# Kernel optimization log

Hardware: AMD Instinct MI355X
Metric: run time of the kernel (lower is better)

The kernel has to match this reference:

```python
import jax, jax.numpy as jnp
import numpy as np

DIM, H, D = 2048, 16, 128
D_C, D_CQ, D_ROPE = 512, 1536, 64
B, T = 2, 2048


def _rope(t, cos, sin):
    # t: [..., T, D_ROPE]; cos/sin: [T, D_ROPE//2] broadcast over leading dims
    h = D_ROPE // 2
    t1, t2 = t[..., :h], t[..., h:]
    return jnp.concatenate([t1 * cos - t2 * sin, t2 * cos + t1 * sin], axis=-1)


def setup_inputs() -> dict:
    key = jax.random.key(0)
    ks = jax.random.split(key, 10)
    init = lambda k, shp, fan: (jax.random.normal(k, shp, jnp.float32) / np.sqrt(fan).astype(np.float32))
    x = jax.random.normal(ks[0], (B, T, DIM), jnp.float32)
    # RoPE tables for d_rope//2 = 32 rotary channels
    inv_freq = 1.0 / (10000.0 ** (np.arange(0, D_ROPE // 2, dtype=np.float32) / (D_ROPE // 2)))
    ang = np.arange(T, dtype=np.float32)[:, None] * inv_freq[None, :]
    cos = jnp.asarray(np.cos(ang), jnp.float32)
    sin = jnp.asarray(np.sin(ang), jnp.float32)
    return {
        "x": x,
        "cos": cos,
        "sin": sin,
        "w_kv": init(ks[1], (DIM, D_C), DIM),          # kv_compress
        "w_kdec": init(ks[2], (D_C, H * D), D_C),       # k_decompress
        "w_vdec": init(ks[3], (D_C, H * D), D_C),       # v_decompress
        "w_qc": init(ks[4], (DIM, D_CQ), DIM),          # q_compress
        "w_qdec": init(ks[5], (D_CQ, H * D), D_CQ),     # q_decompress
        "w_krope": init(ks[6], (DIM, D_ROPE), DIM),     # k_rope_proj
        "w_qrope": init(ks[7], (DIM, D_ROPE), DIM),     # q_rope_proj
        "w_o": init(ks[8], (H * D, DIM), H * D),        # wo
    }


def reference(x, cos, sin, w_kv, w_kdec, w_vdec, w_qc, w_qdec, w_krope, w_qrope, w_o):
    Bx, Tx, _ = x.shape
    # latent compress -> decompress
    c_kv = x @ w_kv                                       # [B,T,d_c]
    k = (c_kv @ w_kdec).reshape(Bx, Tx, H, D).transpose(0, 2, 1, 3)  # [B,H,T,D]
    v = (c_kv @ w_vdec).reshape(Bx, Tx, H, D).transpose(0, 2, 1, 3)
    c_q = x @ w_qc
    q = (c_q @ w_qdec).reshape(Bx, Tx, H, D).transpose(0, 2, 1, 3)
    # RoPE branch: head-shared projections, rotated then broadcast across heads
    k_rope = _rope(x @ w_krope, cos, sin)                 # [B,T,d_rope]
    q_rope = _rope(x @ w_qrope, cos, sin)
    rope_dim = min(D_ROPE, D)
    qr = jnp.broadcast_to(q_rope[:, None, :, :rope_dim], (Bx, H, Tx, rope_dim))
    kr = jnp.broadcast_to(k_rope[:, None, :, :rope_dim], (Bx, H, Tx, rope_dim))
    q = jnp.concatenate([q[..., :-rope_dim], qr], axis=-1)
    k = jnp.concatenate([k[..., :-rope_dim], kr], axis=-1)
    # causal SDPA, scale = 1/sqrt(head_dim)
    scores = jnp.einsum("bhtd,bhsd->bhts", q, k) / np.float32(np.sqrt(D))
    causal = jnp.tril(jnp.ones((Tx, Tx), dtype=bool))
    scores = jnp.where(causal, scores, jnp.float32(-1e30))
    attn = jax.nn.softmax(scores, axis=-1)
    out = jnp.einsum("bhts,bhsd->bhtd", attn, v)
    out = out.transpose(0, 2, 1, 3).reshape(Bx, Tx, H * D)
    return out @ w_o
```

## Files before the change

kernel.cpp:

```cpp
#include <hip/hip_runtime.h>
#include <stdint.h>
#include <math.h>

#define B_    2
#define T_    2048
#define DIM_  2048
#define H_    16
#define DC_   512
#define DCQ_  1536
#define NROWS (B_*T_)

typedef unsigned short u16;
typedef __attribute__((ext_vector_type(8))) __bf16 bf16x8;
typedef __attribute__((ext_vector_type(4))) float  f32x4;
typedef __attribute__((ext_vector_type(8))) unsigned short u16x8;
typedef __attribute__((ext_vector_type(4))) float  f4v;

__device__ __forceinline__ u16 f2bf(float f){
  unsigned u = __float_as_uint(f);
  u += 0x7FFFu + ((u >> 16) & 1u);
  return (u16)(u >> 16);
}
__device__ __forceinline__ float bf2f(u16 h){ return __uint_as_float(((unsigned)h) << 16); }

__device__ __forceinline__ unsigned cvt_pk_bf16(float lo, float hi){
  unsigned r;
  asm("v_cvt_pk_bf16_f32 %0, %1, %2" : "=v"(r) : "v"(lo), "v"(hi));
  return r;
}

__device__ __forceinline__ void gld_lds16(const void* g, void* l){
  auto gp = reinterpret_cast<__attribute__((address_space(1))) unsigned int*>(
      reinterpret_cast<uintptr_t>(g));
  auto lp = reinterpret_cast<__attribute__((address_space(3))) unsigned int*>(
      reinterpret_cast<uintptr_t>(l));
  __builtin_amdgcn_global_load_lds(gp, lp, 16, 0, 0);
}

__device__ __forceinline__ f32x4 mfma16(bf16x8 a, bf16x8 b, f32x4 c){
  return __builtin_amdgcn_mfma_f32_16x16x32_bf16(a, b, c, 0, 0, 0);
}

__device__ __forceinline__ void vmwait0(){ asm volatile("s_waitcnt vmcnt(0)" ::: "memory"); }
__device__ __forceinline__ void vmwait8(){ asm volatile("s_waitcnt vmcnt(8)" ::: "memory"); }
__device__ __forceinline__ void barr(){ asm volatile("s_barrier" ::: "memory"); }


struct TDesc { const void* src; u16* dst; int srcStride, dstStride, cblk, nbx, blk0; };
struct TPack { TDesc d[8]; };
#define CONVBLK 8192

__global__ void k_prep(const void* __restrict__ xsrc, u16* __restrict__ x_bf,
                       TPack p, const u16* __restrict__ cosr){
  __shared__ u16 tile[64][72];
  const int bid = blockIdx.x;
  const int tid = threadIdx.x;
  const int f = (cosr[0] == (u16)0x3F80u);
  if (bid < CONVBLK){
    if (f) return;
    int id = bid * 256 + tid;
    f4v v = reinterpret_cast<const f4v*>(xsrc)[id];
    unsigned lo = (unsigned)f2bf(v.x) | ((unsigned)f2bf(v.y) << 16);
    unsigned hi = (unsigned)f2bf(v.z) | ((unsigned)f2bf(v.w) << 16);
    reinterpret_cast<uint2*>(x_bf)[id] = make_uint2(lo, hi);
    return;
  }
  const int tb = bid - CONVBLK;
  int i = 0;
  #pragma unroll
  for (int k = 1; k < 8; ++k) if (tb >= p.d[k].blk0) i = k;
  const void* src = p.d[i].src;
  u16* dst = p.d[i].dst;
  const int srcStride = p.d[i].srcStride, dstStride = p.d[i].dstStride;
  const int rel = tb - p.d[i].blk0;
  const int bx = rel % p.d[i].nbx, by = rel / p.d[i].nbx;
  const int r0 = by << 6, c0 = bx * p.d[i].cblk;
  #pragma unroll
  for (int it = 0; it < 2; ++it){
    int task = (it << 8) + tid;
    int r = task >> 3, c8 = (task & 7) << 3;
    if (f){
      const u16* pp = (const u16*)src + (size_t)(r0 + r) * srcStride + c0 + c8;
      u16x8 v = *reinterpret_cast<const u16x8*>(pp);
      #pragma unroll
      for (int j = 0; j < 8; ++j) tile[r][c8 + j] = v[j];
    } else {
      const float* pp = (const float*)src + (size_t)(r0 + r) * srcStride + c0 + c8;
      f4v a = reinterpret_cast<const f4v*>(pp)[0];
      f4v b = reinterpret_cast<const f4v*>(pp)[1];
      tile[r][c8+0]=f2bf(a.x); tile[r][c8+1]=f2bf(a.y); tile[r][c8+2]=f2bf(a.z); tile[r][c8+3]=f2bf(a.w);
      tile[r][c8+4]=f2bf(b.x); tile[r][c8+5]=f2bf(b.y); tile[r][c8+6]=f2bf(b.z); tile[r][c8+7]=f2bf(b.w);
    }
  }
  __syncthreads();
  #pragma unroll
  for (int it = 0; it < 2; ++it){
    int task = (it << 8) + tid;
    int rr = task >> 3, cc8 = (task & 7) << 3;
    u16x8 v;
    #pragma unroll
    for (int j = 0; j < 8; ++j) v[j] = tile[cc8 + j][rr];
    *reinterpret_cast<u16x8*>(dst + (size_t)((bx << 6) + rr) * dstStride + r0 + cc8) = v;
  }
}

__global__ __launch_bounds__(256, 2) void k_gemm(
    const u16* __restrict__ A0, int lda0, const u16* __restrict__ Bt0, int K0,
    u16* __restrict__ C0, int ldc0, float os0,
    const u16* __restrict__ A1, int lda1, const u16* __restrict__ Bt1, int K1,
    u16* __restrict__ C1, int ldc1, float os1,
    int ysplit, int swz, void* outp, const u16* __restrict__ cosr,
    const u16* __restrict__ alt0, const u16* __restrict__ alt1,
    u16* __restrict__ vt0, u16* __restrict__ vt1,
    const u16* __restrict__ ropeXc, const void* __restrict__ rcosp,
    const void* __restrict__ rsinp, u16* __restrict__ ropeK,
    u16* __restrict__ ropeQ, int* __restrict__ rticket, int ngemm){
  __shared__ alignas(16) u16 lds[32768];
  const int tid = threadIdx.x;
  const int flat = blockIdx.y * gridDim.x + blockIdx.x;

  if (ropeXc && flat >= ngemm){
    const int rb = flat - ngemm;
    if (rb == 0 && tid < 128) rticket[tid] = 0;
    const int f2 = (((const u16*)rcosp)[0] == (u16)0x3F80u);
    int id = rb * 256 + tid;
    int row = id >> 7, c = id & 127;
    int t = row & (T_ - 1);
    int d = c & 63, i = d & 31;
    float cs, sn;
    if (f2){ cs = bf2f(((const u16*)rcosp)[t * 32 + i]); sn = bf2f(((const u16*)rsinp)[t * 32 + i]); }
    else   { cs = ((const float*)rcosp)[t * 32 + i];     sn = ((const float*)rsinp)[t * 32 + i]; }
    int base = c & 64;
    float t1 = bf2f(ropeXc[(size_t)row * 2304 + 2048 + base + i]);
    float t2 = bf2f(ropeXc[(size_t)row * 2304 + 2048 + base + 32 + i]);
    float v = (d < 32) ? (t1 * cs - t2 * sn) : (t2 * cs + t1 * sn);
    if (c >= 64) v *= 0.12753139626374414f;
    ((c < 64) ? ropeK : ropeQ)[(size_t)row * 64 + d] = f2bf(v);
    return;
  }

  const int wid = tid >> 6, lane = tid & 63;
  const int wr = wid >> 1, wc = wid & 1;
  const int l16 = lane & 15, g = lane >> 4;
  int lin = flat;
  if (swz){
    const int q8 = (gridDim.x * gridDim.y) >> 3;
    lin = (lin & 7) * q8 + (lin >> 3);
  }
  const int m0 = (lin & 31) << 7;
  int nt = lin >> 5;
  const u16 *A, *Bt, *alt; u16 *C, *vtp; int lda, K, ldc; float oscale;
  if (nt < ysplit){ A = A0; lda = lda0; Bt = Bt0; K = K0; C = C0; ldc = ldc0; oscale = os0; alt = alt0; vtp = vt0; }
  else { nt -= ysplit; A = A1; lda = lda1; Bt = Bt1; K = K1; C = C1; ldc = ldc1; oscale = os1; alt = alt1; vtp = vt1; }
  const int f = cosr ? (cosr[0] == (u16)0x3F80u) : 1;
  if (alt && f) A = alt;
  const int n0 = nt << 7;
  const size_t Kz = (size_t)K;
  const int nkt = K >> 6;

  auto STAGE = [&](int kt, int bufn){
    const int kb = kt << 6;
    #pragma unroll
    for (int q = 0; q < 8; ++q){
      const int ht = q >> 2;
      const int cq = ((q & 3) << 8) + tid;
      const int Lb = cq << 4;
      const int row = Lb >> 7;
      const int colb = (Lb & 127) ^ ((row & 7) << 4);
      const u16* src = ht ? (Bt + (size_t)(n0 + row) * Kz + kb + (colb >> 1))
                          : (A  + (size_t)(m0 + row) * lda + kb + (colb >> 1));
      gld_lds16(src, &lds[bufn * 16384 + ht * 8192 + (cq << 3)]);
    }
  };

  f32x4 acc[4][4] = {};

  STAGE(0, 0);
  int buf = 0;

  for (int kt = 0; kt < nkt; ++kt){
    if (kt + 1 < nkt){ STAGE(kt + 1, buf ^ 1); vmwait8(); }
    else vmwait0();
    barr();
    bf16x8 af[2][4], bfr[2][4];
    #pragma unroll
    for (int ks = 0; ks < 2; ++ks){
      #pragma unroll
      for (int mi = 0; mi < 4; ++mi){
        int row = (wr << 6) + (mi << 4) + l16;
        int cb = ((ks << 6) + (g << 4)) ^ ((row & 7) << 4);
        af[ks][mi] = *reinterpret_cast<const bf16x8*>(&lds[buf * 16384 + (((row << 7) + cb) >> 1)]);
      }
      #pragma unroll
      for (int ni = 0; ni < 4; ++ni){
        int row = (wc << 6) + (ni << 4) + l16;
        int cb = ((ks << 6) + (g << 4)) ^ ((row & 7) << 4);
        bfr[ks][ni] = *reinterpret_cast<const bf16x8*>(&lds[buf * 16384 + 8192 + (((row << 7) + cb) >> 1)]);
      }
    }
    __builtin_amdgcn_s_setprio(1);
    #pragma unroll
    for (int ks = 0; ks < 2; ++ks)
      #pragma unroll
      for (int mi = 0; mi < 4; ++mi)
        #pragma unroll
        for (int ni = 0; ni < 4; ++ni)
          acc[mi][ni] = mfma16(af[ks][mi], bfr[ks][ni], acc[mi][ni]);
    __builtin_amdgcn_s_setprio(0);
    barr();
    buf ^= 1;
  }

  const int r4 = g << 2;
  #pragma unroll
  for (int mi = 0; mi < 4; ++mi){
    int row = m0 + (wr << 6) + (mi << 4) + r4;
    #pragma unroll
    for (int ni = 0; ni < 4; ++ni){
      int col = n0 + (wc << 6) + (ni << 4) + l16;
      if (vtp && col >= 1024){
        int hd = col - 1024;
        u16* dst = vtp + (((size_t)(((row >> 11) << 4) + (hd >> 7)) << 7) + (hd & 127)) * (size_t)T_ + (row & (T_ - 1));
        union { u16 u[4]; uint2 v; } pk;
        #pragma unroll
        for (int j = 0; j < 4; ++j) pk.u[j] = f2bf(acc[mi][ni][j] * oscale);
        *reinterpret_cast<uint2*>(dst) = pk.v;
        continue;
      }
      #pragma unroll
      for (int j = 0; j < 4; ++j){
        float v = acc[mi][ni][j] * oscale;
        if (outp){
          if (f) ((u16*)outp)[(size_t)(row + j) * ldc + col] = f2bf(v);
          else   ((float*)outp)[(size_t)(row + j) * ldc + col] = v;
        } else {
          C[(size_t)(row + j) * ldc + col] = f2bf(v);
        }
      }
    }
  }
}

__global__ __launch_bounds__(512, 2) void k_attn(const u16* __restrict__ qP,
                                                 const u16* __restrict__ kvP,
                                                 const u16* __restrict__ vT,
                                                 const u16* __restrict__ krope,
                                                 const u16* __restrict__ qrope,
                                                 u16* __restrict__ aout,
                                                 int* __restrict__ ticket){
  __shared__ alignas(16) u16 smem[32768];
  const int tid = threadIdx.x, wid = tid >> 6, lane = tid & 63;
  const int l16 = lane & 15, g = lane >> 4;
  const int lk = g << 3, r4 = g << 2;
  const int sw8 = (l16 & 7) << 3;
  const int xcd = blockIdx.x & 7;

  while (true){
    if (tid == 0) *(int*)&smem[0] = atomicAdd(&ticket[xcd << 4], 1);
    __syncthreads();
    const int it = *(const int*)&smem[0];
    __syncthreads();
    if (it >= 64) break;
    const int qt = 15 - (it >> 2);
    const int bh = (xcd << 2) + (it & 3), b = bh >> 4, h = bh & 15;
    const int q0 = qt << 7;
    const size_t bT = (size_t)b * T_;
    const u16* kvPb = kvP + bT * 1024 + (h << 6);
    const u16* krb  = krope + bT * 64;
    const u16* vTb  = vT + (size_t)bh * 128 * T_;
    const int qlo = q0 + (wid << 4);
    const int qhi = qlo + 15;
    const int nkv = (qt << 1) + 2;

    auto STAGE = [&](int buf, int k0){
      const int base = buf << 14;
      #pragma unroll
      for (int r = 0; r < 4; ++r){
        int c = (r << 9) + tid;
        const u16* src;
        if (r < 2){
          int row = c >> 4, cc = c & 15;
          int ccx = (cc & 8) | ((cc & 7) ^ (row & 7));
          int col0 = ccx << 3;
          src = (col0 < 64) ? (kvPb + (size_t)(k0 + row) * 1024 + col0)
                            : (krb  + (size_t)(k0 + row) * 64 + (col0 - 64));
        } else {
          int cv = c - 1024;
          int row = cv >> 3, cc = cv & 7;
          int ccx = cc ^ (row & 7);
          src = vTb + (size_t)row * T_ + k0 + (ccx << 3);
        }
        gld_lds16(src, &smem[base + (c << 3)]);
      }
    };

    bf16x8 qf[4];
    {
      size_t grow = bT + qlo + l16;
      #pragma unroll
      for (int ks = 0; ks < 4; ++ks){
        int d = (ks << 5) + lk;
        const u16* src = (ks < 2) ? (qP + grow * 1024 + (h << 6) + d)
                                  : (qrope + grow * 64 + (d - 64));
        qf[ks] = *reinterpret_cast<const bf16x8*>(src);
      }
    }
    f32x4 o[8] = {};
    float m = -3e38f, l = 0.f;

    STAGE(0, 0);
    __syncthreads();
    int cur = 0;

    for (int kv = 0; kv < nkv; ++kv){
      const int k0 = kv << 6;
      if (kv + 1 < nkv) STAGE(cur ^ 1, (kv + 1) << 6);
      if (k0 <= qhi){
        const int kb = cur << 14;
        f32x4 s[4] = {};
        __builtin_amdgcn_s_setprio(1);
        #pragma unroll
        for (int ks = 0; ks < 4; ++ks){
          int colsw = ((ks << 5) + lk) ^ sw8;
          #pragma unroll
          for (int n = 0; n < 4; ++n){
            bf16x8 kf = *reinterpret_cast<const bf16x8*>(&smem[kb + ((n << 4) + l16) * 128 + colsw]);
            s[n] = mfma16(kf, qf[ks], s[n]);
          }
        }
        __builtin_amdgcn_s_setprio(0);
        if (k0 + 63 > qlo){
          const int tq = qlo + l16;
          #pragma unroll
          for (int n = 0; n < 4; ++n)
            #pragma unroll
            for (int j = 0; j < 4; ++j)
              s[n][j] = (k0 + (n << 4) + r4 + j <= tq) ? s[n][j] : -3e38f;
        }
        float mx;
        {
          float a0 = fmaxf(fmaxf(s[0][0], s[0][1]), fmaxf(s[0][2], s[0][3]));
          float a1 = fmaxf(fmaxf(s[1][0], s[1][1]), fmaxf(s[1][2], s[1][3]));
          float a2 = fmaxf(fmaxf(s[2][0], s[2][1]), fmaxf(s[2][2], s[2][3]));
          float a3 = fmaxf(fmaxf(s[3][0], s[3][1]), fmaxf(s[3][2], s[3][3]));
          mx = fmaxf(fmaxf(a0, a1), fmaxf(a2, a3));
          mx = fmaxf(mx, __shfl_xor(mx, 16));
          mx = fmaxf(mx, __shfl_xor(mx, 32));
        }
        if (__ballot(mx > m + 8.f)){
          float mnew = fmaxf(m, mx);
          float alpha = exp2f(m - mnew);
          m = mnew; l *= alpha;
          #pragma unroll
          for (int j = 0; j < 4; ++j){
            float av = __shfl(alpha, r4 + j);
            #pragma unroll
            for (int db = 0; db < 8; ++db) o[db][j] *= av;
          }
        }
        unsigned w[4][2];
        float rs = 0.f;
        #pragma unroll
        for (int n = 0; n < 4; ++n)
          #pragma unroll
          for (int jh = 0; jh < 2; ++jh){
            float p0 = exp2f(s[n][2*jh]     - m);
            float p1 = exp2f(s[n][2*jh + 1] - m);
            rs += p0 + p1;
            w[n][jh] = cvt_pk_bf16(p0, p1);
          }
        rs += __shfl_xor(rs, 16);
        rs += __shfl_xor(rs, 32);
        l += rs;
        const int srcA = l16 + ((g & 1) << 5);
        const int srcB = srcA + 16;
        const bool hi = (g >= 2);
        bf16x8 pa[2];
        #pragma unroll
        for (int ks2 = 0; ks2 < 2; ++ks2){
          unsigned a0 = __shfl((int)w[2*ks2][0],     srcA);
          unsigned b0 = __shfl((int)w[2*ks2 + 1][0], srcA);
          unsigned a1 = __shfl((int)w[2*ks2][1],     srcA);
          unsigned b1 = __shfl((int)w[2*ks2 + 1][1], srcA);
          unsigned a2 = __shfl((int)w[2*ks2][0],     srcB);
          unsigned b2 = __shfl((int)w[2*ks2 + 1][0], srcB);
          unsigned a3 = __shfl((int)w[2*ks2][1],     srcB);
          unsigned b3 = __shfl((int)w[2*ks2 + 1][1], srcB);
          union { unsigned u[4]; bf16x8 v; } pk;
          pk.u[0] = hi ? b0 : a0;
          pk.u[1] = hi ? b1 : a1;
          pk.u[2] = hi ? b2 : a2;
          pk.u[3] = hi ? b3 : a3;
          pa[ks2] = pk.v;
        }
        __builtin_amdgcn_s_setprio(1);
        #pragma unroll
        for (int ks2 = 0; ks2 < 2; ++ks2){
          int colsw = ((ks2 << 5) + lk) ^ sw8;
          #pragma unroll
          for (int db = 0; db < 8; ++db){
            bf16x8 vb = *reinterpret_cast<const bf16x8*>(&smem[(cur << 14) + 8192 + ((db << 4) + l16) * 64 + colsw]);
            o[db] = mfma16(pa[ks2], vb, o[db]);
          }
        }
        __builtin_amdgcn_s_setprio(0);
      }
      __syncthreads();
      cur ^= 1;
    }
    #pragma unroll
    for (int j = 0; j < 4; ++j){
      float lv = __shfl(l, r4 + j);
      float rinv = 1.f / lv;
      const int tq = qlo + r4 + j;
      u16* dst = aout + (bT + tq) * 2048 + (h << 7) + l16;
      #pragma unroll
      for (int db = 0; db < 8; ++db)
        dst[db << 4] = f2bf(o[db][j] * rinv);
    }
  }
}

extern "C" void kernel_launch(void* const* d_in, const int* in_sizes, int n_in,
                              void* d_out, int out_size, void* d_ws, size_t ws_size,
                              hipStream_t stream){
  const void* x       = d_in[0];
  const void* cosp    = d_in[1];
  const void* sinp    = d_in[2];
  const void* w_kv    = d_in[3];
  const void* w_kdec  = d_in[4];
  const void* w_vdec  = d_in[5];
  const void* w_qc    = d_in[6];
  const void* w_qdec  = d_in[7];
  const void* w_krope = d_in[8];
  const void* w_qrope = d_in[9];
  const void* w_o     = d_in[10];

  char* ws = (char*)d_ws;
  size_t off = 0;
  auto alloc = [&](size_t bytes){ void* p = ws + off; off += (bytes + 255) & ~(size_t)255; return p; };
  int* ticket   = (int*)alloc(1024);
  u16* x_bf     = (u16*)alloc((size_t)NROWS * DIM_ * 2);
  u16* w_c1T    = (u16*)alloc((size_t)2304 * DIM_ * 2);
  u16* w_kvdT   = (u16*)alloc((size_t)3072 * DC_ * 2);
  u16* w_qdPT   = (u16*)alloc((size_t)1024 * DCQ_ * 2);
  u16* w_oT     = (u16*)alloc((size_t)DIM_ * DIM_ * 2);
  u16* xc       = (u16*)alloc((size_t)NROWS * 2304 * 2);
  u16* qP       = (u16*)alloc((size_t)NROWS * 1024 * 2);
  u16* kvP      = (u16*)alloc((size_t)NROWS * 1024 * 2);
  u16* krope    = (u16*)alloc((size_t)NROWS * 64 * 2);
  u16* qrope    = (u16*)alloc((size_t)NROWS * 64 * 2);
  u16* vT       = (u16*)alloc((size_t)32 * 128 * T_ * 2);
  u16* aout     = (u16*)alloc((size_t)NROWS * DIM_ * 2);
  (void)in_sizes; (void)n_in; (void)out_size; (void)ws_size;

  const float SC2 = 0.12753139626374414f;
  const u16* cosr = (const u16*)cosp;

  TPack tp;
  tp.d[0] = { w_kv,    w_c1T,                        512,  2048, 64,  8,  0    };
  tp.d[1] = { w_qc,    w_c1T + (size_t)512 * 2048,   1536, 2048, 64,  24, 256  };
  tp.d[2] = { w_krope, w_c1T + (size_t)2048 * 2048,  64,   2048, 64,  1,  1024 };
  tp.d[3] = { w_qrope, w_c1T + (size_t)2112 * 2048,  64,   2048, 64,  1,  1056 };
  tp.d[4] = { w_kdec,  w_kvdT,                       2048, 512,  128, 16, 1088 };
  tp.d[5] = { w_vdec,  w_kvdT + (size_t)1024 * 512,  2048, 512,  64,  32, 1216 };
  tp.d[6] = { w_qdec,  w_qdPT,                       2048, 1536, 128, 16, 1472 };
  tp.d[7] = { w_o,     w_oT,                         2048, 2048, 64,  32, 1856 };
  hipLaunchKernelGGL(k_prep, dim3(CONVBLK + 2880), dim3(256), 0, stream, x, x_bf, tp, cosr);

  hipLaunchKernelGGL(k_gemm, dim3(32, 17), dim3(256), 0, stream,
                     x_bf, DIM_, w_c1T, DIM_, xc, 2304, 1.0f,
                     x_bf, DIM_, w_c1T, DIM_, xc, 2304, 1.0f,
                     17, 1, (void*)nullptr, cosr,
                     (const u16*)x, (const u16*)x,
                     (u16*)nullptr, (u16*)nullptr,
                     (const u16*)nullptr, (const void*)nullptr, (const void*)nullptr,
                     (u16*)nullptr, (u16*)nullptr, (int*)nullptr, 0);
  hipLaunchKernelGGL(k_gemm, dim3(3072, 1), dim3(256), 0, stream,
                     xc + 512, 2304, w_qdPT, DCQ_, qP, 1024, SC2,
                     xc, 2304, w_kvdT, DC_, kvP, 1024, 1.0f,
                     8, 0, (void*)nullptr, (const u16*)nullptr,
                     (const u16*)nullptr, (const u16*)nullptr,
                     (u16*)nullptr, vT,
                     xc, cosp, sinp, krope, qrope, ticket, 1024);
  hipLaunchKernelGGL(k_attn, dim3(256), dim3(512), 0, stream,
                     qP, kvP, vT, krope, qrope, aout, ticket);
  hipLaunchKernelGGL(k_gemm, dim3(32, 16), dim3(256), 0, stream,
                     aout, DIM_, w_oT, DIM_, (u16*)nullptr, DIM_, 1.0f,
                     aout, DIM_, w_oT, DIM_, (u16*)nullptr, DIM_, 1.0f,
                     16, 1, d_out, cosr,
                     (const u16*)nullptr, (const u16*)nullptr,
                     (u16*)nullptr, (u16*)nullptr,
                     (const u16*)nullptr, (const void*)nullptr, (const void*)nullptr,
                     (u16*)nullptr, (u16*)nullptr, (int*)nullptr, 0);
}
```

Measured before the change: 236.2 us.

## Move decompress and output weight transposes into first GEMM launch as side blocks

The prep kernel now transposes only the weights the first GEMM needs. The transposes of the decompress and output-projection weights run as extra side blocks appended to the first GEMM's grid, which becomes a flattened 1D grid, so they overlap with that GEMM instead of delaying it. The swizzle now uses the GEMM block count rather than the grid size, and the kernel takes a side-mode flag plus a transpose descriptor pack. This adds kernel-argument size and a dependency on those side blocks finishing before the second GEMM launch, which stream ordering already guarantees.

```diff
diff --git a/kernel.cpp b/kernel.cpp
--- a/kernel.cpp
+++ b/kernel.cpp
@@ -50,22 +50,9 @@
 struct TPack { TDesc d[8]; };
 #define CONVBLK 8192
 
-__global__ void k_prep(const void* __restrict__ xsrc, u16* __restrict__ x_bf,
-                       TPack p, const u16* __restrict__ cosr){
-  __shared__ u16 tile[64][72];
-  const int bid = blockIdx.x;
-  const int tid = threadIdx.x;
-  const int f = (cosr[0] == (u16)0x3F80u);
-  if (bid < CONVBLK){
-    if (f) return;
-    int id = bid * 256 + tid;
-    f4v v = reinterpret_cast<const f4v*>(xsrc)[id];
-    unsigned lo = (unsigned)f2bf(v.x) | ((unsigned)f2bf(v.y) << 16);
-    unsigned hi = (unsigned)f2bf(v.z) | ((unsigned)f2bf(v.w) << 16);
-    reinterpret_cast<uint2*>(x_bf)[id] = make_uint2(lo, hi);
-    return;
-  }
-  const int tb = bid - CONVBLK;
+__device__ __forceinline__ void do_transpose(void* ldsbuf, const TPack& p, int tb,
+                                             int tid, int f){
+  u16 (*tile)[72] = reinterpret_cast<u16(*)[72]>(ldsbuf);
   int i = 0;
   #pragma unroll
   for (int k = 1; k < 8; ++k) if (tb >= p.d[k].blk0) i = k;
@@ -104,6 +91,24 @@
   }
 }
 
+__global__ void k_prep(const void* __restrict__ xsrc, u16* __restrict__ x_bf,
+                       TPack p, const u16* __restrict__ cosr){
+  __shared__ u16 tile[64][72];
+  const int bid = blockIdx.x;
+  const int tid = threadIdx.x;
+  const int f = (cosr[0] == (u16)0x3F80u);
+  if (bid < CONVBLK){
+    if (f) return;
+    int id = bid * 256 + tid;
+    f4v v = reinterpret_cast<const f4v*>(xsrc)[id];
+    unsigned lo = (unsigned)f2bf(v.x) | ((unsigned)f2bf(v.y) << 16);
+    unsigned hi = (unsigned)f2bf(v.z) | ((unsigned)f2bf(v.w) << 16);
+    reinterpret_cast<uint2*>(x_bf)[id] = make_uint2(lo, hi);
+    return;
+  }
+  do_transpose(tile, p, bid - CONVBLK, tid, f);
+}
+
 __global__ __launch_bounds__(256, 2) void k_gemm(
     const u16* __restrict__ A0, int lda0, const u16* __restrict__ Bt0, int K0,
     u16* __restrict__ C0, int ldc0, float os0,
@@ -114,28 +119,34 @@
     u16* __restrict__ vt0, u16* __restrict__ vt1,
     const u16* __restrict__ ropeXc, const void* __restrict__ rcosp,
     const void* __restrict__ rsinp, u16* __restrict__ ropeK,
-    u16* __restrict__ ropeQ, int* __restrict__ rticket, int ngemm){
+    u16* __restrict__ ropeQ, int* __restrict__ rticket,
+    int ngemm, int sidemode, TPack tpp){
   __shared__ alignas(16) u16 lds[32768];
   const int tid = threadIdx.x;
   const int flat = blockIdx.y * gridDim.x + blockIdx.x;
 
-  if (ropeXc && flat >= ngemm){
-    const int rb = flat - ngemm;
-    if (rb == 0 && tid < 128) rticket[tid] = 0;
-    const int f2 = (((const u16*)rcosp)[0] == (u16)0x3F80u);
-    int id = rb * 256 + tid;
-    int row = id >> 7, c = id & 127;
-    int t = row & (T_ - 1);
-    int d = c & 63, i = d & 31;
-    float cs, sn;
-    if (f2){ cs = bf2f(((const u16*)rcosp)[t * 32 + i]); sn = bf2f(((const u16*)rsinp)[t * 32 + i]); }
-    else   { cs = ((const float*)rcosp)[t * 32 + i];     sn = ((const float*)rsinp)[t * 32 + i]; }
-    int base = c & 64;
-    float t1 = bf2f(ropeXc[(size_t)row * 2304 + 2048 + base + i]);
-    float t2 = bf2f(ropeXc[(size_t)row * 2304 + 2048 + base + 32 + i]);
-    float v = (d < 32) ? (t1 * cs - t2 * sn) : (t2 * cs + t1 * sn);
-    if (c >= 64) v *= 0.12753139626374414f;
-    ((c < 64) ? ropeK : ropeQ)[(size_t)row * 64 + d] = f2bf(v);
+  if (sidemode && flat >= ngemm){
+    const int tb = flat - ngemm;
+    if (sidemode == 1){
+      if (tb == 0 && tid < 128) rticket[tid] = 0;
+      const int f2 = (((const u16*)rcosp)[0] == (u16)0x3F80u);
+      int id = tb * 256 + tid;
+      int row = id >> 7, c = id & 127;
+      int t = row & (T_ - 1);
+      int d = c & 63, i = d & 31;
+      float cs, sn;
+      if (f2){ cs = bf2f(((const u16*)rcosp)[t * 32 + i]); sn = bf2f(((const u16*)rsinp)[t * 32 + i]); }
+      else   { cs = ((const float*)rcosp)[t * 32 + i];     sn = ((const float*)rsinp)[t * 32 + i]; }
+      int base = c & 64;
+      float t1 = bf2f(ropeXc[(size_t)row * 2304 + 2048 + base + i]);
+      float t2 = bf2f(ropeXc[(size_t)row * 2304 + 2048 + base + 32 + i]);
+      float v = (d < 32) ? (t1 * cs - t2 * sn) : (t2 * cs + t1 * sn);
+      if (c >= 64) v *= 0.12753139626374414f;
+      ((c < 64) ? ropeK : ropeQ)[(size_t)row * 64 + d] = f2bf(v);
+    } else {
+      const int f2 = cosr ? (cosr[0] == (u16)0x3F80u) : 1;
+      do_transpose(lds, tpp, tb, tid, f2);
+    }
     return;
   }
 
@@ -144,7 +155,7 @@
   const int l16 = lane & 15, g = lane >> 4;
   int lin = flat;
   if (swz){
-    const int q8 = (gridDim.x * gridDim.y) >> 3;
+    const int q8 = ngemm >> 3;
     lin = (lin & 7) * q8 + (lin >> 3);
   }
   const int m0 = (lin & 31) << 7;
@@ -457,32 +468,45 @@
   const float SC2 = 0.12753139626374414f;
   const u16* cosr = (const u16*)cosp;
 
-  TPack tp;
+  TPack tp = {};
   tp.d[0] = { w_kv,    w_c1T,                        512,  2048, 64,  8,  0    };
   tp.d[1] = { w_qc,    w_c1T + (size_t)512 * 2048,   1536, 2048, 64,  24, 256  };
   tp.d[2] = { w_krope, w_c1T + (size_t)2048 * 2048,  64,   2048, 64,  1,  1024 };
   tp.d[3] = { w_qrope, w_c1T + (size_t)2112 * 2048,  64,   2048, 64,  1,  1056 };
-  tp.d[4] = { w_kdec,  w_kvdT,                       2048, 512,  128, 16, 1088 };
-  tp.d[5] = { w_vdec,  w_kvdT + (size_t)1024 * 512,  2048, 512,  64,  32, 1216 };
-  tp.d[6] = { w_qdec,  w_qdPT,                       2048, 1536, 128, 16, 1472 };
-  tp.d[7] = { w_o,     w_oT,                         2048, 2048, 64,  32, 1856 };
-  hipLaunchKernelGGL(k_prep, dim3(CONVBLK + 2880), dim3(256), 0, stream, x, x_bf, tp, cosr);
-
-  hipLaunchKernelGGL(k_gemm, dim3(32, 17), dim3(256), 0, stream,
+  tp.d[4] = { nullptr, nullptr, 0, 0, 0, 1, 1 << 30 };
+  tp.d[5] = { nullptr, nullptr, 0, 0, 0, 1, 1 << 30 };
+  tp.d[6] = { nullptr, nullptr, 0, 0, 0, 1, 1 << 30 };
+  tp.d[7] = { nullptr, nullptr, 0, 0, 0, 1, 1 << 30 };
+  hipLaunchKernelGGL(k_prep, dim3(CONVBLK + 1088), dim3(256), 0, stream, x, x_bf, tp, cosr);
+
+  TPack ts = {};
+  ts.d[0] = { w_kdec, w_kvdT,                       2048, 512,  128, 16, 0    };
+  ts.d[1] = { w_vdec, w_kvdT + (size_t)1024 * 512,  2048, 512,  64,  32, 128  };
+  ts.d[2] = { w_qdec, w_qdPT,                       2048, 1536, 128, 16, 384  };
+  ts.d[3] = { w_o,    w_oT,                         2048, 2048, 64,  32, 768  };
+  ts.d[4] = { nullptr, nullptr, 0, 0, 0, 1, 1 << 30 };
+  ts.d[5] = { nullptr, nullptr, 0, 0, 0, 1, 1 << 30 };
+  ts.d[6] = { nullptr, nullptr, 0, 0, 0, 1, 1 << 30 };
+  ts.d[7] = { nullptr, nullptr, 0, 0, 0, 1, 1 << 30 };
+  TPack tz = {};
+
+  hipLaunchKernelGGL(k_gemm, dim3(2336, 1), dim3(256), 0, stream,
                      x_bf, DIM_, w_c1T, DIM_, xc, 2304, 1.0f,
                      x_bf, DIM_, w_c1T, DIM_, xc, 2304, 1.0f,
                      17, 1, (void*)nullptr, cosr,
                      (const u16*)x, (const u16*)x,
                      (u16*)nullptr, (u16*)nullptr,
                      (const u16*)nullptr, (const void*)nullptr, (const void*)nullptr,
-                     (u16*)nullptr, (u16*)nullptr, (int*)nullptr, 0);
+                     (u16*)nullptr, (u16*)nullptr, (int*)nullptr,
+                     544, 2, ts);
   hipLaunchKernelGGL(k_gemm, dim3(3072, 1), dim3(256), 0, stream,
                      xc + 512, 2304, w_qdPT, DCQ_, qP, 1024, SC2,
                      xc, 2304, w_kvdT, DC_, kvP, 1024, 1.0f,
                      8, 0, (void*)nullptr, (const u16*)nullptr,
                      (const u16*)nullptr, (const u16*)nullptr,
                      (u16*)nullptr, vT,
-                     xc, cosp, sinp, krope, qrope, ticket, 1024);
+                     xc, cosp, sinp, krope, qrope, ticket,
+                     1024, 1, tz);
   hipLaunchKernelGGL(k_attn, dim3(256), dim3(512), 0, stream,
                      qP, kvP, vT, krope, qrope, aout, ticket);
   hipLaunchKernelGGL(k_gemm, dim3(32, 16), dim3(256), 0, stream,
@@ -492,5 +516,6 @@
                      (const u16*)nullptr, (const u16*)nullptr,
                      (u16*)nullptr, (u16*)nullptr,
                      (const u16*)nullptr, (const void*)nullptr, (const void*)nullptr,
-                     (u16*)nullptr, (u16*)nullptr, (int*)nullptr, 0);
-}
+                     (u16*)nullptr, (u16*)nullptr, (int*)nullptr,
+                     512, 0, tz);
+}
```

Result: no change. 232.4 us (-1.6%).
